# Kernel tuning notes

Hardware: AMD Instinct MI355X
Metric: run time of the kernel (lower is better)

The kernel has to match this reference:

```python
import jax, jax.numpy as jnp
import numpy as np

N = 20000; E = 320000; IN = 128; H = 6; C = 64; HC = H * C; NC = 16; NG = 64


def _gatv2(x, src, dst, wl, bl, wr, br, att, bias, heads, out_c, concat):
    # PyG GATv2Conv (eval mode, share_weights=False, negative_slope=0.2)
    n = x.shape[0]
    xl = (x @ wl + bl).reshape(n, heads, out_c)   # source-side transform
    xr = (x @ wr + br).reshape(n, heads, out_c)   # target-side transform
    # edge-wise attention logits: leaky_relu(x_l[j] + x_r[i]) . att
    e = jnp.einsum('ehc,hc->eh', jax.nn.leaky_relu(xl[src] + xr[dst], 0.2), att)
    # segment softmax over incoming edges of each target node
    emax = jax.ops.segment_max(e, dst, num_segments=n)
    a = jnp.exp(e - emax[dst])
    denom = jax.ops.segment_sum(a, dst, num_segments=n)
    alpha = a / (denom[dst] + 1e-16)
    out = jax.ops.segment_sum(xl[src] * alpha[:, :, None], dst, num_segments=n)
    out = out.reshape(n, heads * out_c) if concat else out.mean(axis=1)
    return out + bias


def setup_inputs() -> dict:
    key = jax.random.key(0)
    ks = jax.random.split(key, 32)
    s = 0.05
    inp = {}
    inp['x'] = jax.random.normal(ks[0], (N, IN), jnp.float32)
    inp['edge_index'] = jax.random.randint(ks[1], (2, E), 0, N, dtype=jnp.int32)
    inp['batch'] = jnp.sort(jax.random.randint(ks[2], (N,), 0, NG, dtype=jnp.int32))
    # input projection (input_dim != hidden_dim * n_heads)
    inp['inp_w'] = jax.random.normal(ks[3], (IN, HC), jnp.float32) * s
    inp['inp_b'] = jnp.zeros((HC,), jnp.float32)
    # layer 0: IN -> (H, C), concat
    inp['l0_wl'] = jax.random.normal(ks[4], (IN, HC), jnp.float32) * s
    inp['l0_bl'] = jnp.zeros((HC,), jnp.float32)
    inp['l0_wr'] = jax.random.normal(ks[5], (IN, HC), jnp.float32) * s
    inp['l0_br'] = jnp.zeros((HC,), jnp.float32)
    inp['l0_att'] = jax.random.normal(ks[6], (H, C), jnp.float32) * s
    inp['l0_bias'] = jnp.zeros((HC,), jnp.float32)
    # layer 1: HC -> (H, C), concat
    inp['l1_wl'] = jax.random.normal(ks[7], (HC, HC), jnp.float32) * s
    inp['l1_bl'] = jnp.zeros((HC,), jnp.float32)
    inp['l1_wr'] = jax.random.normal(ks[8], (HC, HC), jnp.float32) * s
    inp['l1_br'] = jnp.zeros((HC,), jnp.float32)
    inp['l1_att'] = jax.random.normal(ks[9], (H, C), jnp.float32) * s
    inp['l1_bias'] = jnp.zeros((HC,), jnp.float32)
    # layer 2: HC -> (1, C), no concat (mean over the single head)
    inp['l2_wl'] = jax.random.normal(ks[10], (HC, C), jnp.float32) * s
    inp['l2_bl'] = jnp.zeros((C,), jnp.float32)
    inp['l2_wr'] = jax.random.normal(ks[11], (HC, C), jnp.float32) * s
    inp['l2_br'] = jnp.zeros((C,), jnp.float32)
    inp['l2_att'] = jax.random.normal(ks[12], (1, C), jnp.float32) * s
    inp['l2_bias'] = jnp.zeros((C,), jnp.float32)
    # residual projection HC -> C at the last layer (bias-free Linear)
    inp['res_w'] = jax.random.normal(ks[13], (HC, C), jnp.float32) * s
    # dense head: Linear(C,C) + BatchNorm1d(eval) + ReLU + Linear(C,NC)
    inp['d1_w'] = jax.random.normal(ks[14], (C, C), jnp.float32) * s
    inp['d1_b'] = jnp.zeros((C,), jnp.float32)
    inp['bn_g'] = jnp.ones((C,), jnp.float32)
    inp['bn_b'] = jnp.zeros((C,), jnp.float32)
    inp['bn_m'] = jnp.zeros((C,), jnp.float32)
    inp['bn_v'] = jnp.ones((C,), jnp.float32)
    inp['d2_w'] = jax.random.normal(ks[15], (C, NC), jnp.float32) * s
    inp['d2_b'] = jnp.zeros((NC,), jnp.float32)
    return inp


def reference(x, edge_index, batch, inp_w, inp_b,
              l0_wl, l0_bl, l0_wr, l0_br, l0_att, l0_bias,
              l1_wl, l1_bl, l1_wr, l1_br, l1_att, l1_bias,
              l2_wl, l2_bl, l2_wr, l2_br, l2_att, l2_bias,
              res_w, d1_w, d1_b, bn_g, bn_b, bn_m, bn_v, d2_w, d2_b):
    n = x.shape[0]
    sl = jnp.arange(n, dtype=edge_index.dtype)           # self-loops (PyG default)
    src = jnp.concatenate([edge_index[0], sl])
    dst = jnp.concatenate([edge_index[1], sl])
    x_res = x @ inp_w + inp_b
    h = jax.nn.elu(_gatv2(x, src, dst, l0_wl, l0_bl, l0_wr, l0_br, l0_att, l0_bias, H, C, True)) + x_res
    x_res = h
    h = jax.nn.elu(_gatv2(h, src, dst, l1_wl, l1_bl, l1_wr, l1_br, l1_att, l1_bias, H, C, True)) + x_res
    x_res = h
    h = jax.nn.elu(_gatv2(h, src, dst, l2_wl, l2_bl, l2_wr, l2_br, l2_att, l2_bias, 1, C, False)) + x_res @ res_w
    pooled = jax.ops.segment_sum(h, batch, num_segments=NG)
    z = pooled @ d1_w + d1_b
    z = (z - bn_m) / jnp.sqrt(bn_v + 1e-5) * bn_g + bn_b  # BatchNorm1d eval
    z = jax.nn.relu(z) @ d2_w + d2_b
    return h, z
```

## Files before the change

### kernel.cpp

```cpp
#include <hip/hip_runtime.h>
#include <hip/hip_bf16.h>
#include <math.h>

#define NN 20000
#define EE 320000
#define IND 128
#define HH 6
#define CC 64
#define HCC 384
#define NCC 16
#define NGG 64

typedef __bf16 bf16x8 __attribute__((ext_vector_type(8)));
typedef float f32x4 __attribute__((ext_vector_type(4)));
typedef float f32x2 __attribute__((ext_vector_type(2)));
typedef unsigned short ushort_t;
typedef unsigned int uint_t;

#define LOG2E 1.44269504088896f

__device__ inline ushort_t f2bf(float f) {
    union { float f; uint_t u; } x; x.f = f;
    uint_t r = (x.u + 0x7FFF + ((x.u >> 16) & 1)) >> 16;
    return (ushort_t)r;
}
__device__ inline void bf8cvt2(uint4 v, f32x2* f) {
    union { uint_t u; float x; } a, b;
    a.u = v.x << 16; b.u = v.x & 0xFFFF0000u; f[0] = (f32x2){a.x, b.x};
    a.u = v.y << 16; b.u = v.y & 0xFFFF0000u; f[1] = (f32x2){a.x, b.x};
    a.u = v.z << 16; b.u = v.z & 0xFFFF0000u; f[2] = (f32x2){a.x, b.x};
    a.u = v.w << 16; b.u = v.w & 0xFFFF0000u; f[3] = (f32x2){a.x, b.x};
}

template <int CTRL>
__device__ inline float dppadd(float x) {
    int y = __builtin_amdgcn_mov_dpp(__builtin_bit_cast(int, x), CTRL, 0xF, 0xF, true);
    return x + __builtin_bit_cast(float, y);
}

__device__ inline void load_lds16(const ushort_t* g, ushort_t* l) {
    __builtin_amdgcn_global_load_lds(
        (const __attribute__((address_space(1))) void*)g,
        (__attribute__((address_space(3))) void*)l, 16, 0, 0);
}

__device__ inline int xcd_swz(int lin, int nwg) {
    int q = nwg >> 3, r = nwg & 7;
    int xc = lin & 7, j = lin >> 3;
    return (xc < r ? xc * (q + 1) : r * (q + 1) + (xc - r) * q) + j;
}


__global__ void zero_init_kernel(int* counts, int* srcs_tail,
                                 float* pooled, int n, int np) {
    int t = blockIdx.x * blockDim.x + threadIdx.x;
    if (t < n) counts[t] = 0;
    if (t < np) pooled[t] = 0.0f;
    if (t < 8) srcs_tail[t] = 0;
}

__global__ void count_kernel(const int* __restrict__ ei, int* __restrict__ counts, int E) {
    int t = blockIdx.x * blockDim.x + threadIdx.x;
    if (t < E) atomicAdd(&counts[ei[E + t]], 1);
}

__global__ __launch_bounds__(256) void scan_local_kernel(
    const int* __restrict__ counts, int* __restrict__ offsets,
    int* __restrict__ blockSums, int n) {
    __shared__ int lp[256];
    int t = threadIdx.x, b = blockIdx.x;
    int i = b * 256 + t;
    int v = (i < n) ? counts[i] + 1 : 0;
    lp[t] = v;
    __syncthreads();
    for (int o = 1; o < 256; o <<= 1) {
        int u = (t >= o) ? lp[t - o] : 0;
        __syncthreads();
        lp[t] += u;
        __syncthreads();
    }
    if (t == 255) blockSums[b] = lp[255];
    if (i < n) offsets[i] = lp[t] - v;
}

__global__ __launch_bounds__(256) void scan_fixup_kernel(
    const int* __restrict__ blockSums,
    int* __restrict__ offsets, int* __restrict__ cursor, int n, int nb) {
    __shared__ int red[256];
    int t = threadIdx.x, b = blockIdx.x;
    red[t] = (t < b) ? blockSums[t] : 0;
    __syncthreads();
    for (int o = 128; o > 0; o >>= 1) {
        if (t < o) red[t] += red[t + o];
        __syncthreads();
    }
    int prefix = red[0];
    int i = b * 256 + t;
    if (i < n) {
        int val = offsets[i] + prefix;
        offsets[i] = val;
        cursor[i] = val;
    }
    if (b == nb - 1 && t == 0) offsets[n] = prefix + blockSums[b];
}

__global__ void fill_kernel(const int* __restrict__ ei, int* __restrict__ cursor,
                            int* __restrict__ srcs, int E, int n) {
    int t = blockIdx.x * blockDim.x + threadIdx.x;
    if (t < E) {
        int s = ei[t];
        int d = ei[E + t];
        int slot = atomicAdd(&cursor[d], 1);
        srcs[slot] = s << 8;
    } else if (t < E + n) {
        int i = t - E;
        int slot = atomicAdd(&cursor[i], 1);
        srcs[slot] = i << 8;
    }
}

#define WBIG (1152 * IND)
#define WC1 (768 * HCC)
#define WC2 (192 * HCC)
#define XB_N (NN * IND)
#define PREP_TOTAL (WBIG + WC1 + WC2 + XB_N + 1152 + 768 + 192)

__global__ void prep_kernel(const float* __restrict__ x, const float* __restrict__ inp_w,
    const float* __restrict__ l0wl, const float* __restrict__ l0wr,
    const float* __restrict__ l1wl, const float* __restrict__ l1wr,
    const float* __restrict__ l2wl, const float* __restrict__ l2wr,
    const float* __restrict__ resw,
    const float* __restrict__ inp_b,
    const float* __restrict__ l0bl, const float* __restrict__ l0br,
    const float* __restrict__ l1bl, const float* __restrict__ l1br,
    const float* __restrict__ l2bl, const float* __restrict__ l2br,
    ushort_t* wBig, ushort_t* wC1, ushort_t* wC2, ushort_t* xb,
    float* bBig, float* bC1, float* bC2)
{
    int i = blockIdx.x * blockDim.x + threadIdx.x;
    if (i >= PREP_TOTAL) return;
    if (i < WBIG) {
        int col = i >> 7, k = i & 127;
        float v;
        if (col < 384)      v = inp_w[k * 384 + col];
        else if (col < 768) v = l0wl[k * 384 + (col - 384)];
        else                v = l0wr[k * 384 + (col - 768)];
        wBig[i] = f2bf(v); return;
    }
    i -= WBIG;
    if (i < WC1) {
        int col = i / 384, k = i - col * 384;
        float v = col < 384 ? l1wl[k * 384 + col] : l1wr[k * 384 + (col - 384)];
        wC1[i] = f2bf(v); return;
    }
    i -= WC1;
    if (i < WC2) {
        int col = i / 384, k = i - col * 384;
        float v;
        if (col < 64)       v = resw[k * 64 + col];
        else if (col < 128) v = l2wl[k * 64 + (col - 64)];
        else                v = l2wr[k * 64 + (col - 128)];
        wC2[i] = f2bf(v); return;
    }
    i -= WC2;
    if (i < XB_N) { xb[i] = f2bf(x[i]); return; }
    i -= XB_N;
    if (i < 1152) {
        float v;
        if (i < 384)      v = inp_b[i];
        else if (i < 768) v = l0bl[i - 384];
        else              v = l0br[i - 768];
        bBig[i] = v; return;
    }
    i -= 1152;
    if (i < 768) { bC1[i] = i < 384 ? l1bl[i] : l1br[i - 384]; return; }
    i -= 768;
    if (i < 192) {
        float v;
        if (i < 64)       v = 0.0f;
        else if (i < 128) v = l2bl[i - 64];
        else              v = l2br[i - 128];
        bC2[i] = v; return;
    }
}

__global__ __launch_bounds__(512) void gemm_mfma2(
    const ushort_t* __restrict__ A, const ushort_t* __restrict__ BT,
    const float* __restrict__ bias,
    ushort_t* __restrict__ Cb1, int ld1,
    ushort_t* __restrict__ Cb2, int ld2, int split,
    int M, int N, int K, int NT)
{
    __shared__ ushort_t Bs[2][2][128 * 32];
    int t = threadIdx.x;
    int w = t >> 6, L = t & 63;
    int nwg = gridDim.x * gridDim.y;
    int logical = xcd_swz(blockIdx.y * gridDim.x + blockIdx.x, nwg);
    int bx = logical / gridDim.y;
    int by = logical % gridDim.y;
    int m0 = bx * 256;
    int q = L >> 4, r16 = L & 15;
    int lr = L >> 2;
    int lc = ((L & 3) ^ ((lr >> 1) & 3)) * 8;
    int sw = (q ^ ((r16 >> 1) & 3)) * 8;
    int oB = (w * 16) * 32;

    int rA0 = min(m0 + w * 32 + r16, M - 1);
    int rA1 = min(m0 + w * 32 + 16 + r16, M - 1);
    const ushort_t* pA0base = A + (size_t)rA0 * K + q * 8;
    const ushort_t* pA1base = A + (size_t)rA1 * K + q * 8;

    for (int nt = 0; nt < NT; ++nt) {
        int n0 = (by * NT + nt) * 128;
        int rB = min(n0 + w * 16 + lr, N - 1);
        const ushort_t* gB = BT + (size_t)rB * K + lc;
        const ushort_t* pA0 = pA0base;
        const ushort_t* pA1 = pA1base;

        f32x4 acc[2][8];
#pragma unroll
        for (int a = 0; a < 2; ++a)
#pragma unroll
            for (int b = 0; b < 8; ++b) acc[a][b] = (f32x4){0.f, 0.f, 0.f, 0.f};

        load_lds16(gB, &Bs[0][0][oB]);
        load_lds16(gB + 32, &Bs[0][1][oB]);
        gB += 64;
        bf16x8 a0 = *(const bf16x8*)pA0;
        bf16x8 a2 = *(const bf16x8*)(pA0 + 32);
        bf16x8 a1 = *(const bf16x8*)pA1;
        bf16x8 a3 = *(const bf16x8*)(pA1 + 32);
        pA0 += 64; pA1 += 64;

        int buf = 0;
        for (int k0 = 0; k0 < K; k0 += 64) {
            __syncthreads();
            bool more = (k0 + 64 < K);
            if (more) {
                int nb = buf ^ 1;
                load_lds16(gB, &Bs[nb][0][oB]);
                load_lds16(gB + 32, &Bs[nb][1][oB]);
                gB += 64;
            }
            bf16x8 na0, na1, na2, na3;
            if (more) {
                na0 = *(const bf16x8*)pA0;
                na2 = *(const bf16x8*)(pA0 + 32);
                na1 = *(const bf16x8*)pA1;
                na3 = *(const bf16x8*)(pA1 + 32);
                pA0 += 64; pA1 += 64;
            }
#pragma unroll
            for (int ct = 0; ct < 8; ++ct) {
                bf16x8 blo = *(const bf16x8*)&Bs[buf][0][(ct * 16 + r16) * 32 + sw];
                bf16x8 bhi = *(const bf16x8*)&Bs[buf][1][(ct * 16 + r16) * 32 + sw];
                acc[0][ct] = __builtin_amdgcn_mfma_f32_16x16x32_bf16(blo, a0, acc[0][ct], 0, 0, 0);
                acc[1][ct] = __builtin_amdgcn_mfma_f32_16x16x32_bf16(blo, a1, acc[1][ct], 0, 0, 0);
                acc[0][ct] = __builtin_amdgcn_mfma_f32_16x16x32_bf16(bhi, a2, acc[0][ct], 0, 0, 0);
                acc[1][ct] = __builtin_amdgcn_mfma_f32_16x16x32_bf16(bhi, a3, acc[1][ct], 0, 0, 0);
            }
            if (more) { a0 = na0; a1 = na1; a2 = na2; a3 = na3; }
            buf ^= 1;
        }
#pragma unroll
        for (int rt = 0; rt < 2; ++rt) {
            int row = m0 + w * 32 + rt * 16 + r16;
            if (row >= M) continue;
#pragma unroll
            for (int ct = 0; ct < 8; ++ct) {
                int colb = n0 + ct * 16 + q * 4;
                if (colb >= N) continue;
                float4 bv = *(const float4*)(bias + colb);
                uint2 pk;
                pk.x = (uint_t)f2bf(acc[rt][ct][0] + bv.x) | ((uint_t)f2bf(acc[rt][ct][1] + bv.y) << 16);
                pk.y = (uint_t)f2bf(acc[rt][ct][2] + bv.z) | ((uint_t)f2bf(acc[rt][ct][3] + bv.w) << 16);
                if (colb < split)
                    *(uint2*)(Cb1 + (size_t)row * ld1 + colb) = pk;
                else
                    *(uint2*)(Cb2 + (size_t)row * ld2 + (colb - split)) = pk;
            }
        }
    }
}

__global__ __launch_bounds__(256) void gemm_mfma(
    const ushort_t* __restrict__ A, const ushort_t* __restrict__ BT,
    const float* __restrict__ bias,
    float* __restrict__ Cf, ushort_t* __restrict__ Cb1, int ld1,
    ushort_t* __restrict__ Cb2, int ld2, int split,
    int M, int N, int K)
{
    __shared__ ushort_t Bs[2][2][128 * 32];
    int t = threadIdx.x;
    int w = t >> 6, L = t & 63;
    int nwg = gridDim.x * gridDim.y;
    int logical = xcd_swz(blockIdx.y * gridDim.x + blockIdx.x, nwg);
    int m0 = (logical / gridDim.y) * 128;
    int n0 = (logical % gridDim.y) * 128;
    int q = L >> 4, r16 = L & 15;

    f32x4 acc[2][8];
#pragma unroll
    for (int a = 0; a < 2; ++a)
#pragma unroll
        for (int b = 0; b < 8; ++b) acc[a][b] = (f32x4){0.f, 0.f, 0.f, 0.f};

    int lr = L >> 2;
    int lc = ((L & 3) ^ ((lr >> 1) & 3)) * 8;
    int rB0 = min(n0 + w * 32 + lr, N - 1);
    int rB1 = min(n0 + w * 32 + 16 + lr, N - 1);
    const ushort_t* gB0 = BT + (size_t)rB0 * K + lc;
    const ushort_t* gB1 = BT + (size_t)rB1 * K + lc;
    int oB0 = (w * 32) * 32;
    int oB1 = (w * 32 + 16) * 32;

    int rA0 = min(m0 + w * 32 + r16, M - 1);
    int rA1 = min(m0 + w * 32 + 16 + r16, M - 1);
    const ushort_t* pA0 = A + (size_t)rA0 * K + q * 8;
    const ushort_t* pA1 = A + (size_t)rA1 * K + q * 8;

    int sw = (q ^ ((r16 >> 1) & 3)) * 8;

    load_lds16(gB0, &Bs[0][0][oB0]);
    load_lds16(gB1, &Bs[0][0][oB1]);
    load_lds16(gB0 + 32, &Bs[0][1][oB0]);
    load_lds16(gB1 + 32, &Bs[0][1][oB1]);
    gB0 += 64; gB1 += 64;
    bf16x8 a0 = *(const bf16x8*)pA0;
    bf16x8 a2 = *(const bf16x8*)(pA0 + 32);
    bf16x8 a1 = *(const bf16x8*)pA1;
    bf16x8 a3 = *(const bf16x8*)(pA1 + 32);
    pA0 += 64; pA1 += 64;

    int buf = 0;
    for (int k0 = 0; k0 < K; k0 += 64) {
        __syncthreads();
        bool more = (k0 + 64 < K);
        if (more) {
            int nb = buf ^ 1;
            load_lds16(gB0, &Bs[nb][0][oB0]);
            load_lds16(gB1, &Bs[nb][0][oB1]);
            load_lds16(gB0 + 32, &Bs[nb][1][oB0]);
            load_lds16(gB1 + 32, &Bs[nb][1][oB1]);
            gB0 += 64; gB1 += 64;
        }
        bf16x8 na0, na1, na2, na3;
        if (more) {
            na0 = *(const bf16x8*)pA0;
            na2 = *(const bf16x8*)(pA0 + 32);
            na1 = *(const bf16x8*)pA1;
            na3 = *(const bf16x8*)(pA1 + 32);
            pA0 += 64; pA1 += 64;
        }
#pragma unroll
        for (int ct = 0; ct < 8; ++ct) {
            bf16x8 blo = *(const bf16x8*)&Bs[buf][0][(ct * 16 + r16) * 32 + sw];
            bf16x8 bhi = *(const bf16x8*)&Bs[buf][1][(ct * 16 + r16) * 32 + sw];
            acc[0][ct] = __builtin_amdgcn_mfma_f32_16x16x32_bf16(blo, a0, acc[0][ct], 0, 0, 0);
            acc[1][ct] = __builtin_amdgcn_mfma_f32_16x16x32_bf16(blo, a1, acc[1][ct], 0, 0, 0);
            acc[0][ct] = __builtin_amdgcn_mfma_f32_16x16x32_bf16(bhi, a2, acc[0][ct], 0, 0, 0);
            acc[1][ct] = __builtin_amdgcn_mfma_f32_16x16x32_bf16(bhi, a3, acc[1][ct], 0, 0, 0);
        }
        if (more) { a0 = na0; a1 = na1; a2 = na2; a3 = na3; }
        buf ^= 1;
    }
#pragma unroll
    for (int rt = 0; rt < 2; ++rt) {
        int row = m0 + w * 32 + rt * 16 + r16;
        if (row >= M) continue;
#pragma unroll
        for (int ct = 0; ct < 8; ++ct) {
            int colb = n0 + ct * 16 + q * 4;
            if (colb >= N) continue;
            float4 bv = *(const float4*)(bias + colb);
            float v0 = acc[rt][ct][0] + bv.x;
            float v1 = acc[rt][ct][1] + bv.y;
            float v2 = acc[rt][ct][2] + bv.z;
            float v3 = acc[rt][ct][3] + bv.w;
            if (colb < split) {
                if (Cf) {
                    *(float4*)(Cf + (size_t)row * ld1 + colb) = make_float4(v0, v1, v2, v3);
                } else {
                    uint2 pk;
                    pk.x = (uint_t)f2bf(v0) | ((uint_t)f2bf(v1) << 16);
                    pk.y = (uint_t)f2bf(v2) | ((uint_t)f2bf(v3) << 16);
                    *(uint2*)(Cb1 + (size_t)row * ld1 + colb) = pk;
                }
            } else {
                uint2 pk;
                pk.x = (uint_t)f2bf(v0) | ((uint_t)f2bf(v1) << 16);
                pk.y = (uint_t)f2bf(v2) | ((uint_t)f2bf(v3) << 16);
                *(uint2*)(Cb2 + (size_t)row * ld2 + (colb - split)) = pk;
            }
        }
    }
}

__global__ __launch_bounds__(128) void gat6_kernel(
    const ushort_t* __restrict__ cat, const float* __restrict__ att,
    const float* __restrict__ bias, const ushort_t* __restrict__ resB,
    ushort_t* __restrict__ outB,
    const int* __restrict__ offsets, const int* __restrict__ srcs, int n)
{
    int wid = (blockIdx.x * blockDim.x + threadIdx.x) >> 6;
    if (wid >= n) return;
    int lane = threadIdx.x & 63;
    int h = lane >> 3, c8 = lane & 7;
    bool hv = h < HH;
    int off = h * 64 + c8 * 8;
    int offL2 = (hv ? off : off - 384) * 2;
    int i = wid;
    int beg = __builtin_amdgcn_readfirstlane(offsets[i]);
    int end = __builtin_amdgcn_readfirstlane(offsets[i + 1]);
    int deg = end - beg;
    int P = (deg + 1) >> 1;
    const char* catc = (const char*)cat;

    f32x2 xr2[4], att2[4];
    {
        uint4 v = *(const uint4*)(catc + (size_t)i * 1536 + 768 + offL2);
        bf8cvt2(v, xr2);
    }
#pragma unroll
    for (int j = 0; j < 4; ++j) {
        int o = (offL2 >> 1) + 2 * j;
        att2[j] = (f32x2){att[o] * LOG2E, att[o + 1] * LOG2E};
    }

    float s = 0.0f;
    f32x2 acc2[4];
#pragma unroll
    for (int j = 0; j < 4; ++j) acc2[j] = (f32x2){0.f, 0.f};

    int bA0 = srcs[beg] * 6, bB0 = srcs[beg + 1] * 6;
    uint4 cA = *(const uint4*)(catc + (size_t)(uint_t)bA0 + offL2);
    uint4 cB = *(const uint4*)(catc + (size_t)(uint_t)bB0 + offL2);
    int iA1 = srcs[beg + 2] * 6, iB1 = srcs[beg + 3] * 6;

    for (int p = 0; p < P; ++p) {
        uint4 nA = cA, nB = cB;
        bool pre = (p + 1 < P);
        if (pre) {
            nA = *(const uint4*)(catc + (size_t)(uint_t)iA1 + offL2);
            nB = *(const uint4*)(catc + (size_t)(uint_t)iB1 + offL2);
            iA1 = srcs[beg + 2 * p + 4] * 6;
            iB1 = srcs[beg + 2 * p + 5] * 6;
        }
        f32x2 xlA[4], xlB[4];
        bf8cvt2(cA, xlA);
        bf8cvt2(cB, xlB);
        f32x2 pA2 = (f32x2){0.f, 0.f}, pB2 = (f32x2){0.f, 0.f};
#pragma unroll
        for (int j = 0; j < 4; ++j) {
            f32x2 ta = xlA[j] + xr2[j];
            ta = __builtin_elementwise_max(ta, ta * 0.2f);
            pA2 += ta * att2[j];
            f32x2 tb = xlB[j] + xr2[j];
            tb = __builtin_elementwise_max(tb, tb * 0.2f);
            pB2 += tb * att2[j];
        }
        float pA = pA2.x + pA2.y, pB = pB2.x + pB2.y;
        pA = dppadd<0xB1>(pA);
        pB = dppadd<0xB1>(pB);
        pA = dppadd<0x4E>(pA);
        pB = dppadd<0x4E>(pB);
        pA = dppadd<0x141>(pA);
        pB = dppadd<0x141>(pB);
        float wA = __builtin_amdgcn_exp2f(pA);
        float wB = (2 * p + 1 < deg) ? __builtin_amdgcn_exp2f(pB) : 0.0f;
        s += wA + wB;
        f32x2 wA2 = (f32x2){wA, wA}, wB2 = (f32x2){wB, wB};
#pragma unroll
        for (int j = 0; j < 4; ++j) {
            acc2[j] += wA2 * xlA[j];
            acc2[j] += wB2 * xlB[j];
        }
        cA = nA; cB = nB;
    }

    if (hv) {
        float inv = 1.0f / (s + 1e-16f);
        size_t ob = (size_t)i * HCC + off;
        uint4 rv = *(const uint4*)(resB + ob);
        f32x2 rr[4];
        bf8cvt2(rv, rr);
        ushort_t u[8];
#pragma unroll
        for (int j = 0; j < 4; ++j) {
            float v0 = acc2[j].x * inv + bias[off + 2 * j];
            float v1 = acc2[j].y * inv + bias[off + 2 * j + 1];
            v0 = v0 > 0.0f ? v0 : expm1f(v0);
            v1 = v1 > 0.0f ? v1 : expm1f(v1);
            u[2 * j]     = f2bf(v0 + rr[j].x);
            u[2 * j + 1] = f2bf(v1 + rr[j].y);
        }
        *(uint4*)(outB + ob) = *(uint4*)u;
    }
}

__global__ __launch_bounds__(128) void gat1_kernel(
    const ushort_t* __restrict__ cat, const float* __restrict__ att,
    const float* __restrict__ bias, const float* __restrict__ res,
    float* __restrict__ out,
    const int* __restrict__ offsets, const int* __restrict__ srcs, int n)
{
    int wid = (blockIdx.x * blockDim.x + threadIdx.x) >> 6;
    if (wid >= n) return;
    int lane = threadIdx.x & 63;
    int e8 = lane >> 3, c8 = lane & 7;
    int i = wid;
    int beg = __builtin_amdgcn_readfirstlane(offsets[i]);
    int end = __builtin_amdgcn_readfirstlane(offsets[i + 1]);
    const char* catc = (const char*)cat;

    f32x2 xr2[4], att2[4];
    {
        uint4 v = *(const uint4*)(cat + (size_t)i * 128 + 64 + c8 * 8);
        bf8cvt2(v, xr2);
    }
#pragma unroll
    for (int j = 0; j < 4; ++j)
        att2[j] = (f32x2){att[c8 * 8 + 2 * j] * LOG2E, att[c8 * 8 + 2 * j + 1] * LOG2E};

    float s = 0.0f;
    f32x2 acc2[4];
#pragma unroll
    for (int j = 0; j < 4; ++j) acc2[j] = (f32x2){0.f, 0.f};

    const uint4 z = make_uint4(0u, 0u, 0u, 0u);
    int p = beg + e8;
    bool val = p < end;
    int b = val ? srcs[p] : (i << 8);
    uint4 v = *(const uint4*)(catc + (size_t)(uint_t)b + c8 * 16);

    for (int p0 = beg; p0 < end; p0 += 8) {
        uint4 nv = z;
        bool nval = false;
        if (p0 + 8 < end) {
            int np = p0 + 8 + e8;
            nval = np < end;
            int nb = nval ? srcs[np] : (i << 8);
            nv = *(const uint4*)(catc + (size_t)(uint_t)nb + c8 * 16);
        }
        f32x2 xl[4];
        bf8cvt2(v, xl);
        f32x2 pp2 = (f32x2){0.f, 0.f};
#pragma unroll
        for (int j = 0; j < 4; ++j) {
            f32x2 tv = xl[j] + xr2[j];
            tv = __builtin_elementwise_max(tv, tv * 0.2f);
            pp2 += tv * att2[j];
        }
        float partial = pp2.x + pp2.y;
        partial = dppadd<0xB1>(partial);
        partial = dppadd<0x4E>(partial);
        partial = dppadd<0x141>(partial);
        float wE = val ? __builtin_amdgcn_exp2f(partial) : 0.0f;
        s += wE;
        f32x2 w2 = (f32x2){wE, wE};
#pragma unroll
        for (int j = 0; j < 4; ++j) acc2[j] += w2 * xl[j];
        v = nv;
        val = nval;
    }

    s = dppadd<0x140>(s);
    s += __shfl_xor(s, 16, 64);
    s += __shfl_xor(s, 32, 64);
#pragma unroll
    for (int j = 0; j < 4; ++j) {
        acc2[j].x += __shfl_xor(acc2[j].x, 8, 64);
        acc2[j].y += __shfl_xor(acc2[j].y, 8, 64);
        acc2[j].x += __shfl_xor(acc2[j].x, 16, 64);
        acc2[j].y += __shfl_xor(acc2[j].y, 16, 64);
        acc2[j].x += __shfl_xor(acc2[j].x, 32, 64);
        acc2[j].y += __shfl_xor(acc2[j].y, 32, 64);
    }
    if (e8 == 0) {
        float inv = 1.0f / (s + 1e-16f);
        size_t ob = (size_t)i * CC + c8 * 8;
        float4 r0 = *(const float4*)(res + ob);
        float4 r1 = *(const float4*)(res + ob + 4);
        float rr[8] = {r0.x, r0.y, r0.z, r0.w, r1.x, r1.y, r1.z, r1.w};
        float av[8] = {acc2[0].x, acc2[0].y, acc2[1].x, acc2[1].y,
                       acc2[2].x, acc2[2].y, acc2[3].x, acc2[3].y};
#pragma unroll
        for (int j = 0; j < 8; ++j) {
            float v2 = av[j] * inv + bias[c8 * 8 + j];
            v2 = v2 > 0.0f ? v2 : expm1f(v2);
            av[j] = v2 + rr[j];
        }
        *(float4*)(out + ob) = make_float4(av[0], av[1], av[2], av[3]);
        *(float4*)(out + ob + 4) = make_float4(av[4], av[5], av[6], av[7]);
    }
}

__global__ __launch_bounds__(256) void pool_kernel(const float* __restrict__ h,
                                                   const int* __restrict__ batch,
                                                   float* __restrict__ pooled, int n) {
    int b = blockIdx.x;
    int g = b >> 2, qd = b & 3;
    int t = threadIdx.x;
    int w = t >> 6, lane = t & 63;
    int lo = 0, hi = n;
    while (lo < hi) { int mid = (lo + hi) >> 1; if (batch[mid] < g) lo = mid + 1; else hi = mid; }
    int start = lo;
    int hi2 = n;
    while (lo < hi2) { int mid = (lo + hi2) >> 1; if (batch[mid] < g + 1) lo = mid + 1; else hi2 = mid; }
    int endd = lo;
    int len = endd - start;
    int q0 = start + (len * qd) / 4;
    int q1 = start + (len * (qd + 1)) / 4;
    float acc = 0.0f;
    for (int r = q0 + w; r < q1; r += 4)
        acc += h[(size_t)r * 64 + lane];
    __shared__ float red[4][64];
    red[w][lane] = acc;
    __syncthreads();
    if (w == 0) {
        float v2 = red[0][lane] + red[1][lane] + red[2][lane] + red[3][lane];
        atomicAdd(&pooled[g * 64 + lane], v2);
    }
}

__global__ __launch_bounds__(256) void head_kernel(const float* __restrict__ pooled,
                            const float* __restrict__ d1w, const float* __restrict__ d1b,
                            const float* __restrict__ bng, const float* __restrict__ bnb,
                            const float* __restrict__ bnm, const float* __restrict__ bnv,
                            const float* __restrict__ d2w, const float* __restrict__ d2b,
                            float* __restrict__ zout) {
    __shared__ float pl[64 * 64];
    __shared__ float w1[64 * 64];
    __shared__ float w2[64 * NCC];
    __shared__ float z1[64 * 64];
    int t = threadIdx.x;
    for (int i = t * 4; i < 64 * 64; i += 1024) {
        *(float4*)&pl[i] = *(const float4*)&pooled[i];
        *(float4*)&w1[i] = *(const float4*)&d1w[i];
    }
    for (int i = t * 4; i < 64 * NCC; i += 1024)
        *(float4*)&w2[i] = *(const float4*)&d2w[i];
    __syncthreads();
    for (int idx = t; idx < 64 * 64; idx += 256) {
        int r = idx >> 6, c = idx & 63;
        float acc = d1b[c];
        for (int k = 0; k < 64; ++k) acc += pl[r * 64 + k] * w1[k * 64 + c];
        acc = (acc - bnm[c]) / sqrtf(bnv[c] + 1e-5f) * bng[c] + bnb[c];
        z1[idx] = acc > 0.0f ? acc : 0.0f;
    }
    __syncthreads();
    for (int idx = t; idx < 64 * NCC; idx += 256) {
        int r = idx >> 4, c = idx & 15;
        float acc = d2b[c];
        for (int k = 0; k < 64; ++k) acc += z1[r * 64 + k] * w2[k * NCC + c];
        zout[idx] = acc;
    }
}


extern "C" void kernel_launch(void* const* d_in, const int* in_sizes, int n_in,
                              void* d_out, int out_size, void* d_ws, size_t ws_size,
                              hipStream_t stream) {
    const int N = NN, E = EE, C = CC, HC = HCC, NG = NGG;
    const int EN = E + N;

    const float* x     = (const float*)d_in[0];
    const int*   ei    = (const int*)d_in[1];
    const int*   batch = (const int*)d_in[2];
    const float* inp_w = (const float*)d_in[3];
    const float* inp_b = (const float*)d_in[4];
    const float* l0_wl = (const float*)d_in[5];
    const float* l0_bl = (const float*)d_in[6];
    const float* l0_wr = (const float*)d_in[7];
    const float* l0_br = (const float*)d_in[8];
    const float* l0_att = (const float*)d_in[9];
    const float* l0_bias = (const float*)d_in[10];
    const float* l1_wl = (const float*)d_in[11];
    const float* l1_bl = (const float*)d_in[12];
    const float* l1_wr = (const float*)d_in[13];
    const float* l1_br = (const float*)d_in[14];
    const float* l1_att = (const float*)d_in[15];
    const float* l1_bias = (const float*)d_in[16];
    const float* l2_wl = (const float*)d_in[17];
    const float* l2_bl = (const float*)d_in[18];
    const float* l2_wr = (const float*)d_in[19];
    const float* l2_br = (const float*)d_in[20];
    const float* l2_att = (const float*)d_in[21];
    const float* l2_bias = (const float*)d_in[22];
    const float* res_w = (const float*)d_in[23];
    const float* d1_w = (const float*)d_in[24];
    const float* d1_b = (const float*)d_in[25];
    const float* bn_g = (const float*)d_in[26];
    const float* bn_b = (const float*)d_in[27];
    const float* bn_m = (const float*)d_in[28];
    const float* bn_v = (const float*)d_in[29];
    const float* d2_w = (const float*)d_in[30];
    const float* d2_b = (const float*)d_in[31];

    float* out = (float*)d_out;

    char* ws = (char*)d_ws;
    size_t off = 0;
    auto alloc = [&](size_t bytes) -> void* {
        void* p = ws + off;
        off += (bytes + 255) & ~(size_t)255;
        return p;
    };
    ushort_t* bufH_b  = (ushort_t*)alloc((size_t)N * HC * 2);
    ushort_t* cat01_b = (ushort_t*)alloc((size_t)N * 768 * 2 + 2048);
    ushort_t* xres_b  = (ushort_t*)alloc((size_t)N * HC * 2);
    ushort_t* cat2_b  = (ushort_t*)alloc((size_t)N * 128 * 2);
    float*    bufRes  = (float*)alloc((size_t)N * C * 4);
    ushort_t* xb      = (ushort_t*)alloc((size_t)N * IND * 2);
    ushort_t* wBig    = (ushort_t*)alloc((size_t)WBIG * 2);
    ushort_t* wC1     = (ushort_t*)alloc((size_t)WC1 * 2);
    ushort_t* wC2     = (ushort_t*)alloc((size_t)WC2 * 2);
    float*    bBig    = (float*)alloc((size_t)1152 * 4);
    float*    bC1     = (float*)alloc((size_t)768 * 4);
    float*    bC2     = (float*)alloc((size_t)192 * 4);
    int*      counts  = (int*)alloc((size_t)N * 4);
    int*      cursor  = (int*)alloc((size_t)N * 4);
    int*      offsets = (int*)alloc((size_t)(N + 1) * 4);
    int*      srcs    = (int*)alloc((size_t)(EN + 8) * 4);
    int*      blockSums = (int*)alloc((size_t)256 * 4);
    float*    pooled  = (float*)alloc((size_t)NG * C * 4);

    const int SCAN_NB = (N + 255) / 256;

    zero_init_kernel<<<(N + 255) / 256, 256, 0, stream>>>(counts, srcs + EN,
                                                          pooled, N, NG * C);
    count_kernel<<<(E + 255) / 256, 256, 0, stream>>>(ei, counts, E);
    scan_local_kernel<<<SCAN_NB, 256, 0, stream>>>(counts, offsets, blockSums, N);
    scan_fixup_kernel<<<SCAN_NB, 256, 0, stream>>>(blockSums, offsets, cursor, N, SCAN_NB);
    fill_kernel<<<(EN + 255) / 256, 256, 0, stream>>>(ei, cursor, srcs, E, N);
    prep_kernel<<<(PREP_TOTAL + 255) / 256, 256, 0, stream>>>(
        x, inp_w, l0_wl, l0_wr, l1_wl, l1_wr, l2_wl, l2_wr, res_w,
        inp_b, l0_bl, l0_br, l1_bl, l1_br, l2_bl, l2_br,
        wBig, wC1, wC2, xb, bBig, bC1, bC2);

    int mtiles256 = (N + 255) / 256;
    int mtiles = (N + 127) / 128;
    dim3 gblk(128);
    int gatBlocks = (N * 64 + 127) / 128;

    gemm_mfma2<<<dim3(mtiles256, 3), dim3(512), 0, stream>>>(xb, wBig, bBig,
        xres_b, HC, cat01_b, 768, 384, N, 1152, IND, 3);
    gat6_kernel<<<gatBlocks, gblk, 0, stream>>>(cat01_b, l0_att, l0_bias,
                                                xres_b, bufH_b, offsets, srcs, N);
    gemm_mfma2<<<dim3(mtiles256, 3), dim3(512), 0, stream>>>(bufH_b, wC1, bC1,
        nullptr, 0, cat01_b, 768, 0, N, 768, HC, 2);
    gat6_kernel<<<gatBlocks, gblk, 0, stream>>>(cat01_b, l1_att, l1_bias,
                                                bufH_b, bufH_b, offsets, srcs, N);
    gemm_mfma<<<dim3(mtiles, 2), dim3(256), 0, stream>>>(bufH_b, wC2, bC2,
        bufRes, nullptr, C, cat2_b, 128, 64, N, 192, HC);
    gat1_kernel<<<gatBlocks, gblk, 0, stream>>>(cat2_b, l2_att, l2_bias,
                                                bufRes, out, offsets, srcs, N);
    pool_kernel<<<NG * 4, 256, 0, stream>>>(out, batch, pooled, N);
    head_kernel<<<1, 256, 0, stream>>>(pooled, d1_w, d1_b, bn_g, bn_b, bn_m, bn_v,
                                       d2_w, d2_b, out + (size_t)N * C);
}
```

Baseline: 394.2 us.

## Unroll GAT edge loop by two and replace big-tile GEMM with 128x128 variant

After: 369.1 us (median of 2 runs). 6.4% less time.

```diff
diff --git a/kernel.cpp b/kernel.cpp
--- a/kernel.cpp
+++ b/kernel.cpp
@@ -56,7 +56,7 @@
     int t = blockIdx.x * blockDim.x + threadIdx.x;
     if (t < n) counts[t] = 0;
     if (t < np) pooled[t] = 0.0f;
-    if (t < 8) srcs_tail[t] = 0;
+    if (t < 32) srcs_tail[t] = 0;
 }
 
 __global__ void count_kernel(const int* __restrict__ ei, int* __restrict__ counts, int E) {
@@ -181,105 +181,6 @@
         else if (i < 128) v = l2bl[i - 64];
         else              v = l2br[i - 128];
         bC2[i] = v; return;
-    }
-}
-
-__global__ __launch_bounds__(512) void gemm_mfma2(
-    const ushort_t* __restrict__ A, const ushort_t* __restrict__ BT,
-    const float* __restrict__ bias,
-    ushort_t* __restrict__ Cb1, int ld1,
-    ushort_t* __restrict__ Cb2, int ld2, int split,
-    int M, int N, int K, int NT)
-{
-    __shared__ ushort_t Bs[2][2][128 * 32];
-    int t = threadIdx.x;
-    int w = t >> 6, L = t & 63;
-    int nwg = gridDim.x * gridDim.y;
-    int logical = xcd_swz(blockIdx.y * gridDim.x + blockIdx.x, nwg);
-    int bx = logical / gridDim.y;
-    int by = logical % gridDim.y;
-    int m0 = bx * 256;
-    int q = L >> 4, r16 = L & 15;
-    int lr = L >> 2;
-    int lc = ((L & 3) ^ ((lr >> 1) & 3)) * 8;
-    int sw = (q ^ ((r16 >> 1) & 3)) * 8;
-    int oB = (w * 16) * 32;
-
-    int rA0 = min(m0 + w * 32 + r16, M - 1);
-    int rA1 = min(m0 + w * 32 + 16 + r16, M - 1);
-    const ushort_t* pA0base = A + (size_t)rA0 * K + q * 8;
-    const ushort_t* pA1base = A + (size_t)rA1 * K + q * 8;
-
-    for (int nt = 0; nt < NT; ++nt) {
-        int n0 = (by * NT + nt) * 128;
-        int rB = min(n0 + w * 16 + lr, N - 1);
-        const ushort_t* gB = BT + (size_t)rB * K + lc;
-        const ushort_t* pA0 = pA0base;
-        const ushort_t* pA1 = pA1base;
-
-        f32x4 acc[2][8];
-#pragma unroll
-        for (int a = 0; a < 2; ++a)
-#pragma unroll
-            for (int b = 0; b < 8; ++b) acc[a][b] = (f32x4){0.f, 0.f, 0.f, 0.f};
-
-        load_lds16(gB, &Bs[0][0][oB]);
-        load_lds16(gB + 32, &Bs[0][1][oB]);
-        gB += 64;
-        bf16x8 a0 = *(const bf16x8*)pA0;
-        bf16x8 a2 = *(const bf16x8*)(pA0 + 32);
-        bf16x8 a1 = *(const bf16x8*)pA1;
-        bf16x8 a3 = *(const bf16x8*)(pA1 + 32);
-        pA0 += 64; pA1 += 64;
-
-        int buf = 0;
-        for (int k0 = 0; k0 < K; k0 += 64) {
-            __syncthreads();
-            bool more = (k0 + 64 < K);
-            if (more) {
-                int nb = buf ^ 1;
-                load_lds16(gB, &Bs[nb][0][oB]);
-                load_lds16(gB + 32, &Bs[nb][1][oB]);
-                gB += 64;
-            }
-            bf16x8 na0, na1, na2, na3;
-            if (more) {
-                na0 = *(const bf16x8*)pA0;
-                na2 = *(const bf16x8*)(pA0 + 32);
-                na1 = *(const bf16x8*)pA1;
-                na3 = *(const bf16x8*)(pA1 + 32);
-                pA0 += 64; pA1 += 64;
-            }
-#pragma unroll
-            for (int ct = 0; ct < 8; ++ct) {
-                bf16x8 blo = *(const bf16x8*)&Bs[buf][0][(ct * 16 + r16) * 32 + sw];
-                bf16x8 bhi = *(const bf16x8*)&Bs[buf][1][(ct * 16 + r16) * 32 + sw];
-                acc[0][ct] = __builtin_amdgcn_mfma_f32_16x16x32_bf16(blo, a0, acc[0][ct], 0, 0, 0);
-                acc[1][ct] = __builtin_amdgcn_mfma_f32_16x16x32_bf16(blo, a1, acc[1][ct], 0, 0, 0);
-                acc[0][ct] = __builtin_amdgcn_mfma_f32_16x16x32_bf16(bhi, a2, acc[0][ct], 0, 0, 0);
-                acc[1][ct] = __builtin_amdgcn_mfma_f32_16x16x32_bf16(bhi, a3, acc[1][ct], 0, 0, 0);
-            }
-            if (more) { a0 = na0; a1 = na1; a2 = na2; a3 = na3; }
-            buf ^= 1;
-        }
-#pragma unroll
-        for (int rt = 0; rt < 2; ++rt) {
-            int row = m0 + w * 32 + rt * 16 + r16;
-            if (row >= M) continue;
-#pragma unroll
-            for (int ct = 0; ct < 8; ++ct) {
-                int colb = n0 + ct * 16 + q * 4;
-                if (colb >= N) continue;
-                float4 bv = *(const float4*)(bias + colb);
-                uint2 pk;
-                pk.x = (uint_t)f2bf(acc[rt][ct][0] + bv.x) | ((uint_t)f2bf(acc[rt][ct][1] + bv.y) << 16);
-                pk.y = (uint_t)f2bf(acc[rt][ct][2] + bv.z) | ((uint_t)f2bf(acc[rt][ct][3] + bv.w) << 16);
-                if (colb < split)
-                    *(uint2*)(Cb1 + (size_t)row * ld1 + colb) = pk;
-                else
-                    *(uint2*)(Cb2 + (size_t)row * ld2 + (colb - split)) = pk;
-            }
-        }
     }
 }
 
@@ -527,41 +428,51 @@
 #pragma unroll
     for (int j = 0; j < 4; ++j) acc2[j] = (f32x2){0.f, 0.f};
 
-    const uint4 z = make_uint4(0u, 0u, 0u, 0u);
-    int p = beg + e8;
-    bool val = p < end;
-    int b = val ? srcs[p] : (i << 8);
-    uint4 v = *(const uint4*)(catc + (size_t)(uint_t)b + c8 * 16);
-
-    for (int p0 = beg; p0 < end; p0 += 8) {
-        uint4 nv = z;
-        bool nval = false;
-        if (p0 + 8 < end) {
-            int np = p0 + 8 + e8;
-            nval = np < end;
-            int nb = nval ? srcs[np] : (i << 8);
-            nv = *(const uint4*)(catc + (size_t)(uint_t)nb + c8 * 16);
-        }
-        f32x2 xl[4];
-        bf8cvt2(v, xl);
-        f32x2 pp2 = (f32x2){0.f, 0.f};
+    int pA = beg + e8, pB = beg + 8 + e8;
+    bool vA = pA < end, vB = pB < end;
+    uint4 a = *(const uint4*)(catc + (size_t)(uint_t)srcs[pA] + c8 * 16);
+    uint4 b = *(const uint4*)(catc + (size_t)(uint_t)srcs[pB] + c8 * 16);
+
+    for (int p0 = beg; p0 < end; p0 += 16) {
+        uint4 na = a, nb = b;
+        bool nvA = false, nvB = false;
+        bool pre = (p0 + 16 < end);
+        if (pre) {
+            int qA = p0 + 16 + e8, qB = p0 + 24 + e8;
+            nvA = qA < end; nvB = qB < end;
+            na = *(const uint4*)(catc + (size_t)(uint_t)srcs[qA] + c8 * 16);
+            nb = *(const uint4*)(catc + (size_t)(uint_t)srcs[qB] + c8 * 16);
+        }
+        f32x2 xlA[4], xlB[4];
+        bf8cvt2(a, xlA);
+        bf8cvt2(b, xlB);
+        f32x2 lA2 = (f32x2){0.f, 0.f}, lB2 = (f32x2){0.f, 0.f};
 #pragma unroll
         for (int j = 0; j < 4; ++j) {
-            f32x2 tv = xl[j] + xr2[j];
-            tv = __builtin_elementwise_max(tv, tv * 0.2f);
-            pp2 += tv * att2[j];
-        }
-        float partial = pp2.x + pp2.y;
-        partial = dppadd<0xB1>(partial);
-        partial = dppadd<0x4E>(partial);
-        partial = dppadd<0x141>(partial);
-        float wE = val ? __builtin_amdgcn_exp2f(partial) : 0.0f;
-        s += wE;
-        f32x2 w2 = (f32x2){wE, wE};
-#pragma unroll
-        for (int j = 0; j < 4; ++j) acc2[j] += w2 * xl[j];
-        v = nv;
-        val = nval;
+            f32x2 ta = xlA[j] + xr2[j];
+            ta = __builtin_elementwise_max(ta, ta * 0.2f);
+            lA2 += ta * att2[j];
+            f32x2 tb = xlB[j] + xr2[j];
+            tb = __builtin_elementwise_max(tb, tb * 0.2f);
+            lB2 += tb * att2[j];
+        }
+        float lA = lA2.x + lA2.y, lB = lB2.x + lB2.y;
+        lA = dppadd<0xB1>(lA);
+        lB = dppadd<0xB1>(lB);
+        lA = dppadd<0x4E>(lA);
+        lB = dppadd<0x4E>(lB);
+        lA = dppadd<0x141>(lA);
+        lB = dppadd<0x141>(lB);
+        float wA = vA ? __builtin_amdgcn_exp2f(lA) : 0.0f;
+        float wB = vB ? __builtin_amdgcn_exp2f(lB) : 0.0f;
+        s += wA + wB;
+        f32x2 wA2 = (f32x2){wA, wA}, wB2 = (f32x2){wB, wB};
+#pragma unroll
+        for (int j = 0; j < 4; ++j) {
+            acc2[j] += wA2 * xlA[j];
+            acc2[j] += wB2 * xlB[j];
+        }
+        a = na; b = nb; vA = nvA; vB = nvB;
     }
 
     s = dppadd<0x140>(s);
@@ -721,7 +632,7 @@
     int*      counts  = (int*)alloc((size_t)N * 4);
     int*      cursor  = (int*)alloc((size_t)N * 4);
     int*      offsets = (int*)alloc((size_t)(N + 1) * 4);
-    int*      srcs    = (int*)alloc((size_t)(EN + 8) * 4);
+    int*      srcs    = (int*)alloc((size_t)(EN + 32) * 4);
     int*      blockSums = (int*)alloc((size_t)256 * 4);
     float*    pooled  = (float*)alloc((size_t)NG * C * 4);
 
@@ -738,17 +649,16 @@
         inp_b, l0_bl, l0_br, l1_bl, l1_br, l2_bl, l2_br,
         wBig, wC1, wC2, xb, bBig, bC1, bC2);
 
-    int mtiles256 = (N + 255) / 256;
     int mtiles = (N + 127) / 128;
     dim3 gblk(128);
     int gatBlocks = (N * 64 + 127) / 128;
 
-    gemm_mfma2<<<dim3(mtiles256, 3), dim3(512), 0, stream>>>(xb, wBig, bBig,
-        xres_b, HC, cat01_b, 768, 384, N, 1152, IND, 3);
+    gemm_mfma<<<dim3(mtiles, 9), dim3(256), 0, stream>>>(xb, wBig, bBig,
+        nullptr, xres_b, HC, cat01_b, 768, 384, N, 1152, IND);
     gat6_kernel<<<gatBlocks, gblk, 0, stream>>>(cat01_b, l0_att, l0_bias,
                                                 xres_b, bufH_b, offsets, srcs, N);
-    gemm_mfma2<<<dim3(mtiles256, 3), dim3(512), 0, stream>>>(bufH_b, wC1, bC1,
-        nullptr, 0, cat01_b, 768, 0, N, 768, HC, 2);
+    gemm_mfma<<<dim3(mtiles, 6), dim3(256), 0, stream>>>(bufH_b, wC1, bC1,
+        nullptr, nullptr, 0, cat01_b, 768, 0, N, 768, HC);
     gat6_kernel<<<gatBlocks, gblk, 0, stream>>>(cat01_b, l1_att, l1_bias,
                                                 bufH_b, bufH_b, offsets, srcs, N);
     gemm_mfma<<<dim3(mtiles, 2), dim3(256), 0, stream>>>(bufH_b, wC2, bC2,
```
